# Optimization experiments

Hardware: AMD Instinct MI355X
Metric: run time of the kernel (lower is better)

The kernel has to match this reference:

```python
import jax, jax.numpy as jnp
import numpy as np

N_HEADS = 12
D_MODEL = 768
D_HEAD = 64
LN_EPS = 1e-5


def setup_inputs() -> dict:
    key = jax.random.key(0)
    ks = jax.random.split(key, 7)
    bs, slen = 1, 4096
    s_in = 1.0 / np.sqrt(D_MODEL)
    s_out = 1.0 / np.sqrt(N_HEADS * D_HEAD)
    return {
        "x": jax.random.normal(ks[0], (bs, slen, D_MODEL), jnp.float32),
        "W_attn": jax.random.uniform(ks[1], (D_MODEL, 3 * N_HEADS * D_HEAD), jnp.float32, -s_in, s_in),
        "b_attn": jax.random.uniform(ks[2], (3 * N_HEADS * D_HEAD,), jnp.float32, -s_in, s_in),
        "W_out": jax.random.uniform(ks[3], (N_HEADS * D_HEAD, D_MODEL), jnp.float32, -s_out, s_out),
        "b_out": jax.random.uniform(ks[4], (D_MODEL,), jnp.float32, -s_out, s_out),
        "ln_g": jnp.ones((D_MODEL,), jnp.float32),
        "ln_b": jnp.zeros((D_MODEL,), jnp.float32),
    }


def reference(x, W_attn, b_attn, W_out, b_out, ln_g, ln_b):
    bs, slen, _ = x.shape
    qkv = x @ W_attn + b_attn                      # [b, s, 3*H*D]
    wq, wk, wv = jnp.split(qkv, 3, axis=-1)
    def to_heads(t):
        return t.reshape(bs, slen, N_HEADS, D_HEAD)
    q, k, v = to_heads(wq), to_heads(wk), to_heads(wv)
    # scores: [b, h, s_q, s_k]
    scores = jnp.einsum('bqhd,bkhd->bhqk', q, k) / np.sqrt(D_HEAD).astype(np.float32)
    probs = jax.nn.softmax(scores, axis=-1)
    attn = jnp.einsum('bhqk,bkhd->bqhd', probs, v).reshape(bs, slen, N_HEADS * D_HEAD)
    out = attn @ W_out + b_out
    y = x + out
    mu = jnp.mean(y, axis=-1, keepdims=True)
    var = jnp.mean(jnp.square(y - mu), axis=-1, keepdims=True)
    return (y - mu) / jnp.sqrt(var + LN_EPS) * ln_g + ln_b
```

## Files before the change

### kernel.cpp

```cpp
#include <hip/hip_runtime.h>
#include <cstdint>
#include <cstddef>

#define SL 4096
#define DM 768

typedef short s16x8 __attribute__((ext_vector_type(8)));
typedef unsigned short u16x8 __attribute__((ext_vector_type(8)));
typedef unsigned short u16x4 __attribute__((ext_vector_type(4)));
typedef float f32x4 __attribute__((ext_vector_type(4)));
typedef float f32x16 __attribute__((ext_vector_type(16)));
typedef unsigned int u32x4 __attribute__((ext_vector_type(4)));

__device__ __forceinline__ unsigned short f2bf(float f) {
  unsigned u = __float_as_uint(f);
  u = u + 0x7fffu + ((u >> 16) & 1u);
  return (unsigned short)(u >> 16);
}

__device__ __forceinline__ int swz(int row, int col) {
  return (row << 6) + ((((col >> 3) ^ row) & 7) << 3) + (col & 7);
}

__device__ __forceinline__ int aswz(int row, int col) {
  return (row << 6) + ((((col >> 3) ^ row ^ (row >> 3)) & 7) << 3) + (col & 7);
}

__device__ __forceinline__ int vswz(int d, int col) {
  return (d << 5) + ((((col >> 3) ^ (d >> 1)) & 3) << 3) + (col & 7);
}

#define ASYNC16(G, L)                                                        \
  __builtin_amdgcn_global_load_lds(                                          \
      (const __attribute__((address_space(1))) void*)(G),                    \
      (__attribute__((address_space(3))) void*)(L), 16, 0, 0)

#define WAITB()                                   \
  do {                                            \
    asm volatile("s_waitcnt vmcnt(0)" ::: "memory"); \
    __builtin_amdgcn_s_barrier();                 \
  } while (0)

__device__ __forceinline__ void tr_body(
    const float* __restrict__ in, unsigned short* __restrict__ out,
    int R, int C, int bx, int by, float (*tile)[65], int t) {
  const int r0 = by * 64, c0 = bx * 64;
  const int lr = t >> 2, lcb = (t & 3) * 16;
  #pragma unroll
  for (int j = 0; j < 16; j += 4) {
    f32x4 v = *reinterpret_cast<const f32x4*>(in + (size_t)(r0 + lr) * C + c0 + lcb + j);
    tile[lr][lcb + j + 0] = v[0];
    tile[lr][lcb + j + 1] = v[1];
    tile[lr][lcb + j + 2] = v[2];
    tile[lr][lcb + j + 3] = v[3];
  }
  __syncthreads();
  #pragma unroll
  for (int j = 0; j < 16; j += 4) {
    u16x4 o;
    o[0] = f2bf(tile[lcb + j + 0][lr]);
    o[1] = f2bf(tile[lcb + j + 1][lr]);
    o[2] = f2bf(tile[lcb + j + 2][lr]);
    o[3] = f2bf(tile[lcb + j + 3][lr]);
    *reinterpret_cast<u16x4*>(out + (size_t)(c0 + lr) * R + r0 + lcb + j) = o;
  }
}

extern "C" __global__ __launch_bounds__(256) void k_prep(
    const float* __restrict__ x, const float* __restrict__ Wa,
    const float* __restrict__ Wo, unsigned short* __restrict__ xbf,
    unsigned short* __restrict__ wat, unsigned short* __restrict__ wot,
    unsigned* __restrict__ kmx) {
  __shared__ float tile[64][65];
  const int b = blockIdx.x, t = threadIdx.x;
  if (b < 3072) {
    if (b == 0 && t < 12) kmx[t] = 0u;
    const int i = (b * 256 + t) * 4;
    f32x4 v = *reinterpret_cast<const f32x4*>(x + i);
    u16x4 o;
    o[0] = f2bf(v[0]); o[1] = f2bf(v[1]); o[2] = f2bf(v[2]); o[3] = f2bf(v[3]);
    *reinterpret_cast<u16x4*>(xbf + i) = o;
  } else if (b < 3504) {
    const int bb = b - 3072;
    tr_body(Wa, wat, 768, 2304, bb % 36, bb / 36, tile, t);
  } else {
    const int bb = b - 3504;
    tr_body(Wo, wot, 768, 768, bb % 12, bb / 12, tile, t);
  }
}

extern "C" __global__ __launch_bounds__(256) void k_qkv(
    const unsigned short* __restrict__ xbf, const unsigned short* __restrict__ wt,
    const float* __restrict__ bias, unsigned short* __restrict__ qb,
    unsigned short* __restrict__ kbo, unsigned short* __restrict__ vtb,
    float* __restrict__ qn2, unsigned* __restrict__ kmx) {
  __shared__ alignas(16) unsigned short a_lds[2][8192];
  __shared__ alignas(16) unsigned short b_lds[2][8192];
  const int t = threadIdx.x, w = t >> 6, l = t & 63;
  const int l15 = l & 15, lg = l >> 4;
  const int wr = w >> 1, wc = w & 1;
  const int n0 = blockIdx.x * 128, m0 = blockIdx.y * 128;
  f32x4 acc[4][4];
  #pragma unroll
  for (int mt = 0; mt < 4; mt++)
    #pragma unroll
    for (int nt = 0; nt < 4; nt++) acc[mt][nt] = (f32x4)0.f;
  int soff[4];
  #pragma unroll
  for (int c = 0; c < 4; c++) {
    int i = c * 256 + t;
    int row = i >> 3, bp = i & 7;
    soff[c] = row * DM + (bp ^ (row & 7)) * 8;
  }
  const unsigned short* asrc = xbf + (size_t)m0 * DM;
  const unsigned short* bsrc = wt + (size_t)n0 * DM;

#define STAGE128(B, KK)                                                   \
  do {                                                                    \
    _Pragma("unroll")                                                     \
    for (int c = 0; c < 4; c++) {                                         \
      ASYNC16(asrc + (KK) + soff[c], &a_lds[B][0] + c * 2048 + w * 512);  \
      ASYNC16(bsrc + (KK) + soff[c], &b_lds[B][0] + c * 2048 + w * 512);  \
    }                                                                     \
  } while (0)

#define GEMM128(B)                                                            \
  do {                                                                        \
    _Pragma("unroll")                                                         \
    for (int kc = 0; kc < 2; kc++) {                                          \
      s16x8 af[4], bfv[4];                                                    \
      _Pragma("unroll")                                                       \
      for (int mt = 0; mt < 4; mt++)                                          \
        af[mt] = *reinterpret_cast<const s16x8*>(                             \
            &a_lds[B][swz(wr * 64 + mt * 16 + l15, kc * 32 + lg * 8)]);       \
      _Pragma("unroll")                                                       \
      for (int nt = 0; nt < 4; nt++)                                          \
        bfv[nt] = *reinterpret_cast<const s16x8*>(                            \
            &b_lds[B][swz(wc * 64 + nt * 16 + l15, kc * 32 + lg * 8)]);       \
      _Pragma("unroll")                                                       \
      for (int mt = 0; mt < 4; mt++)                                          \
        _Pragma("unroll")                                                     \
        for (int nt = 0; nt < 4; nt++)                                        \
          acc[mt][nt] = __builtin_amdgcn_mfma_f32_16x16x32_bf16(              \
              af[mt], bfv[nt], acc[mt][nt], 0, 0, 0);                         \
    }                                                                         \
  } while (0)

  STAGE128(0, 0);
  WAITB();
  #pragma unroll 1
  for (int kk = 0; kk < DM; kk += 128) {
    STAGE128(1, kk + 64);
    GEMM128(0);
    WAITB();
    if (kk + 128 < DM) STAGE128(0, kk + 128);
    GEMM128(1);
    WAITB();
  }
#undef STAGE128
#undef GEMM128

  const int secn = (n0 >= 1536) ? 2 : (n0 >= 768 ? 1 : 0);
  const int nbase = n0 - secn * 768 + wc * 64;
  const int h = nbase >> 6;
  const int mrow0 = m0 + wr * 64;
  float bv4[4];
  #pragma unroll
  for (int nt = 0; nt < 4; nt++) bv4[nt] = bias[secn * 768 + nbase + nt * 16 + l15];

  if (secn == 0) {
    const float QS = 0.180336880f;
    float s2[4][4];
    #pragma unroll
    for (int mt = 0; mt < 4; mt++) {
      #pragma unroll
      for (int r = 0; r < 4; r++) s2[mt][r] = 0.f;
    }
    #pragma unroll
    for (int mt = 0; mt < 4; mt++) {
      #pragma unroll
      for (int nt = 0; nt < 4; nt++) {
        const int d = nt * 16 + l15;
        #pragma unroll
        for (int r = 0; r < 4; r++) {
          const int m = mrow0 + mt * 16 + lg * 4 + r;
          float v = (acc[mt][nt][r] + bv4[nt]) * QS;
          qb[((size_t)h * SL + m) * 64 + d] = f2bf(v);
          s2[mt][r] = fmaf(v, v, s2[mt][r]);
        }
      }
    }
    #pragma unroll
    for (int mt = 0; mt < 4; mt++)
      #pragma unroll
      for (int r = 0; r < 4; r++) {
        #pragma unroll
        for (int off = 1; off < 16; off <<= 1)
          s2[mt][r] += __shfl_xor(s2[mt][r], off, 64);
      }
    if (l15 == 0) {
      #pragma unroll
      for (int mt = 0; mt < 4; mt++)
        #pragma unroll
        for (int r = 0; r < 4; r++)
          qn2[(size_t)h * SL + mrow0 + mt * 16 + lg * 4 + r] = s2[mt][r];
    }
  } else if (secn == 1) {
    float s2[4][4];
    #pragma unroll
    for (int mt = 0; mt < 4; mt++) {
      #pragma unroll
      for (int r = 0; r < 4; r++) s2[mt][r] = 0.f;
    }
    #pragma unroll
    for (int mt = 0; mt < 4; mt++) {
      #pragma unroll
      for (int nt = 0; nt < 4; nt++) {
        const int d = nt * 16 + l15;
        #pragma unroll
        for (int r = 0; r < 4; r++) {
          const int m = mrow0 + mt * 16 + lg * 4 + r;
          float v = acc[mt][nt][r] + bv4[nt];
          kbo[((size_t)h * SL + m) * 64 + d] = f2bf(v);
          s2[mt][r] = fmaf(v, v, s2[mt][r]);
        }
      }
    }
    float rm = 0.f;
    #pragma unroll
    for (int mt = 0; mt < 4; mt++)
      #pragma unroll
      for (int r = 0; r < 4; r++) {
        #pragma unroll
        for (int off = 1; off < 16; off <<= 1)
          s2[mt][r] += __shfl_xor(s2[mt][r], off, 64);
        rm = fmaxf(rm, s2[mt][r]);
      }
    rm = fmaxf(rm, __shfl_xor(rm, 16, 64));
    rm = fmaxf(rm, __shfl_xor(rm, 32, 64));
    if (l == 0) atomicMax(kmx + h, __float_as_uint(rm));
  } else {
    #pragma unroll
    for (int mt = 0; mt < 4; mt++) {
      #pragma unroll
      for (int nt = 0; nt < 4; nt++) {
        const int d = nt * 16 + l15;
        u16x4 o;
        #pragma unroll
        for (int r = 0; r < 4; r++) o[r] = f2bf(acc[mt][nt][r] + bv4[nt]);
        *reinterpret_cast<u16x4*>(
            vtb + ((size_t)h * 64 + d) * SL + mrow0 + mt * 16 + lg * 4) = o;
      }
    }
  }
}

__device__ __forceinline__ void attn_body32f(
    const unsigned short* kb, const unsigned short* vb,
    const s16x8* qf, f32x16* ot, f32x16& lacc, s16x8 qm,
    const int* kfo, const int* vfo, s16x8 ones) {
  f32x16 st = (f32x16)0.f;
  __builtin_amdgcn_s_setprio(1);
  #pragma unroll
  for (int c = 0; c < 4; c++) {
    s16x8 kf = *reinterpret_cast<const s16x8*>(&kb[kfo[c]]);
    st = __builtin_amdgcn_mfma_f32_32x32x16_bf16(kf, qf[c], st, 0, 0, 0);
  }
  st = __builtin_amdgcn_mfma_f32_32x32x16_bf16(ones, qm, st, 0, 0, 0);
  __builtin_amdgcn_s_setprio(0);
  #pragma unroll
  for (int r = 0; r < 16; r++) st[r] = exp2f(st[r]);
  #pragma unroll
  for (int m = 0; m < 2; m++) {
    const int m0 = m * 8;
    unsigned w0, w1, w2, w3;
    asm("v_cvt_pk_bf16_f32 %0, %1, %2" : "=v"(w0) : "v"(st[m0 + 0]), "v"(st[m0 + 1]));
    asm("v_cvt_pk_bf16_f32 %0, %1, %2" : "=v"(w1) : "v"(st[m0 + 2]), "v"(st[m0 + 3]));
    asm("v_cvt_pk_bf16_f32 %0, %1, %2" : "=v"(w2) : "v"(st[m0 + 4]), "v"(st[m0 + 5]));
    asm("v_cvt_pk_bf16_f32 %0, %1, %2" : "=v"(w3) : "v"(st[m0 + 6]), "v"(st[m0 + 7]));
    asm volatile("v_permlane32_swap_b32 %0, %1" : "+v"(w0), "+v"(w2));
    asm volatile("v_permlane32_swap_b32 %0, %1" : "+v"(w1), "+v"(w3));
    u32x4 wv_;
    wv_[0] = w0; wv_[1] = w1; wv_[2] = w2; wv_[3] = w3;
    s16x8 pbf = *reinterpret_cast<s16x8*>(&wv_);
    __builtin_amdgcn_s_setprio(1);
    #pragma unroll
    for (int dt = 0; dt < 2; dt++) {
      s16x8 vf = *reinterpret_cast<const s16x8*>(&vb[vfo[m * 2 + dt]]);
      ot[dt] = __builtin_amdgcn_mfma_f32_32x32x16_bf16(vf, pbf, ot[dt], 0, 0, 0);
    }
    lacc = __builtin_amdgcn_mfma_f32_32x32x16_bf16(ones, pbf, lacc, 0, 0, 0);
    __builtin_amdgcn_s_setprio(0);
  }
}

extern "C" __global__ __launch_bounds__(256) void k_attn(
    const unsigned short* __restrict__ qb, const unsigned short* __restrict__ kbi,
    const unsigned short* __restrict__ vt, const float* __restrict__ qn2,
    const unsigned* __restrict__ kmx, unsigned short* __restrict__ aout) {
  __shared__ alignas(16) unsigned char smem[32768];
  unsigned short* kst = (unsigned short*)smem;
  unsigned short* vst = (unsigned short*)(smem + 16384);
  const int t = threadIdx.x, w = t >> 6, l = t & 63;
  const int l31 = l & 31, s = l >> 5;
  const int half = w >> 1, qs = w & 1;
  const int bid = blockIdx.x;
  const int sid = (bid & 7) * 96 + (bid >> 3);
  const int h = sid >> 6, qt = sid & 63;
  const unsigned short* qh = qb + (size_t)h * SL * 64;
  const unsigned short* kh = kbi + (size_t)h * SL * 64 + (size_t)half * 2048 * 64;
  const unsigned short* vh = vt + (size_t)h * 64 * SL + half * 2048;
  const int q = qt * 64 + qs * 32 + l31;
  const float M = sqrtf(qn2[(size_t)h * SL + q] * __uint_as_float(kmx[h]));
  s16x8 qf[4];
  #pragma unroll
  for (int c = 0; c < 4; c++)
    qf[c] = *reinterpret_cast<const s16x8*>(qh + (size_t)q * 64 + c * 16 + s * 8);
  s16x8 ones;
  #pragma unroll
  for (int e = 0; e < 8; e++) ones[e] = (short)0x3F80;
  s16x8 qm = (s16x8)0;
  if (s == 0) qm[0] = (short)f2bf(-M);
  f32x16 ot[2];
  ot[0] = (f32x16)0.f;
  ot[1] = (f32x16)0.f;
  f32x16 lacc = (f32x16)0.f;
  int koff[2], voff[2];
  #pragma unroll
  for (int c = 0; c < 2; c++) {
    int i = (qs * 2 + c) * 64 + l;
    int key = i >> 3, kb_ = i & 7;
    koff[c] = key * 64 + (kb_ ^ ((key ^ (key >> 3)) & 7)) * 8;
    int d = i >> 2, vb_ = i & 3;
    voff[c] = d * SL + (vb_ ^ ((d >> 1) & 3)) * 8;
  }
  int kfo[4], vfo[4];
  #pragma unroll
  for (int c = 0; c < 4; c++) kfo[c] = aswz(l31, c * 16 + s * 8);
  #pragma unroll
  for (int m = 0; m < 2; m++)
    #pragma unroll
    for (int dt = 0; dt < 2; dt++) vfo[m * 2 + dt] = vswz(dt * 32 + l31, m * 16 + s * 8);

#define STAGE_KV(B, LB)                                                     \
  do {                                                                      \
    _Pragma("unroll")                                                       \
    for (int c = 0; c < 2; c++) {                                           \
      ASYNC16(kh + (size_t)(LB) * 64 + koff[c],                             \
              kst + (half * 2 + (B)) * 2048 + (qs * 2 + c) * 512);          \
      ASYNC16(vh + (LB) + voff[c],                                          \
              vst + (half * 2 + (B)) * 2048 + (qs * 2 + c) * 512);          \
    }                                                                       \
  } while (0)

  STAGE_KV(0, 0);
  WAITB();
  for (int lb = 0; lb < 2048; lb += 64) {
    STAGE_KV(1, lb + 32);
    attn_body32f(kst + (half * 2) * 2048, vst + (half * 2) * 2048,
                 qf, ot, lacc, qm, kfo, vfo, ones);
    WAITB();
    if (lb + 64 < 2048) STAGE_KV(0, lb + 64);
    attn_body32f(kst + (half * 2 + 1) * 2048, vst + (half * 2 + 1) * 2048,
                 qf, ot, lacc, qm, kfo, vfo, ones);
    WAITB();
  }
#undef STAGE_KV
  const float lsum = lacc[0];
  float* o_m = (float*)smem;
  float* l_m = (float*)(smem + 17408);
  __syncthreads();
  if (half == 1) {
    #pragma unroll
    for (int dt = 0; dt < 2; dt++) {
      #pragma unroll
      for (int rq = 0; rq < 4; rq++) {
        f32x4 v;
        #pragma unroll
        for (int j = 0; j < 4; j++) v[j] = ot[dt][rq * 4 + j];
        *reinterpret_cast<f32x4*>(&o_m[(qs * 32 + l31) * 68 + dt * 32 + rq * 8 + s * 4]) = v;
      }
    }
    if (s == 0) l_m[qs * 32 + l31] = lsum;
  }
  __syncthreads();
  if (half == 0) {
    const float linv = 1.f / (lsum + l_m[qs * 32 + l31]);
    #pragma unroll
    for (int dt = 0; dt < 2; dt++) {
      #pragma unroll
      for (int rq = 0; rq < 4; rq++) {
        f32x4 vb_ = *reinterpret_cast<const f32x4*>(&o_m[(qs * 32 + l31) * 68 + dt * 32 + rq * 8 + s * 4]);
        u16x4 o;
        #pragma unroll
        for (int j = 0; j < 4; j++)
          o[j] = f2bf((ot[dt][rq * 4 + j] + vb_[j]) * linv);
        *reinterpret_cast<u16x4*>(aout + (size_t)q * DM + h * 64 + dt * 32 + rq * 8 + s * 4) = o;
      }
    }
  }
}

__device__ __forceinline__ void gemm_body(
    const unsigned short* al, const unsigned short* bl, f32x4* acc,
    int wv, int l15, int lg) {
  #pragma unroll
  for (int kc = 0; kc < 2; kc++) {
    s16x8 af = *reinterpret_cast<const s16x8*>(&al[swz(wv * 16 + l15, kc * 32 + lg * 8)]);
    #pragma unroll
    for (int nt = 0; nt < 4; nt++) {
      s16x8 bfr = *reinterpret_cast<const s16x8*>(&bl[swz(nt * 16 + l15, kc * 32 + lg * 8)]);
      acc[nt] = __builtin_amdgcn_mfma_f32_16x16x32_bf16(af, bfr, acc[nt], 0, 0, 0);
    }
  }
}

extern "C" __global__ __launch_bounds__(256) void k_out(
    const unsigned short* __restrict__ abf, const unsigned short* __restrict__ wot,
    const float* __restrict__ bias, const float* __restrict__ x, float* __restrict__ y) {
  __shared__ alignas(16) unsigned short a_lds[2][4096];
  __shared__ alignas(16) unsigned short b_lds[2][4096];
  const int t = threadIdx.x, wv = t >> 6, l = t & 63;
  const int l15 = l & 15, lg = l >> 4;
  const int m0 = blockIdx.y * 64, n0 = blockIdx.x * 64;
  f32x4 acc[4];
  acc[0] = acc[1] = acc[2] = acc[3] = (f32x4)0.f;
  int soff[2];
  #pragma unroll
  for (int c = 0; c < 2; c++) {
    int idx = wv * 128 + c * 64 + l;
    int row = idx >> 3, bp = idx & 7;
    soff[c] = row * DM + (bp ^ (row & 7)) * 8;
  }
  const unsigned short* asrc = abf + (size_t)m0 * DM;
  const unsigned short* bsrc = wot + (size_t)n0 * DM;
  unsigned short* la = &a_lds[0][0];
  unsigned short* lb = &b_lds[0][0];

#define STAGE_AB(B, KK)                                              \
  do {                                                               \
    ASYNC16(asrc + (KK) + soff[0], la + (B)*4096 + wv * 1024);       \
    ASYNC16(asrc + (KK) + soff[1], la + (B)*4096 + wv * 1024 + 512); \
    ASYNC16(bsrc + (KK) + soff[0], lb + (B)*4096 + wv * 1024);       \
    ASYNC16(bsrc + (KK) + soff[1], lb + (B)*4096 + wv * 1024 + 512); \
  } while (0)

  STAGE_AB(0, 0);
  WAITB();
  for (int kk = 0; kk < DM; kk += 128) {
    STAGE_AB(1, kk + 64);
    gemm_body(&a_lds[0][0], &b_lds[0][0], acc, wv, l15, lg);
    WAITB();
    if (kk + 128 < DM) STAGE_AB(0, kk + 128);
    gemm_body(&a_lds[1][0], &b_lds[1][0], acc, wv, l15, lg);
    WAITB();
  }
#undef STAGE_AB
  const int mb = m0 + wv * 16 + lg * 4;
  #pragma unroll
  for (int nt = 0; nt < 4; nt++) {
    const int n = n0 + nt * 16 + l15;
    const float bv = bias[n];
    #pragma unroll
    for (int r = 0; r < 4; r++)
      y[(size_t)(mb + r) * DM + n] = acc[nt][r] + bv + x[(size_t)(mb + r) * DM + n];
  }
}

extern "C" __global__ __launch_bounds__(256) void k_ln(
    const float* __restrict__ y, const float* __restrict__ g, const float* __restrict__ b,
    float* __restrict__ out) {
  const int row = blockIdx.x, t = threadIdx.x;
  const float* yr = y + (size_t)row * DM;
  float v0 = yr[t], v1 = yr[t + 256], v2 = yr[t + 512];
  float sum = v0 + v1 + v2;
  float sq = v0 * v0 + v1 * v1 + v2 * v2;
  #pragma unroll
  for (int off = 1; off < 64; off <<= 1) {
    sum += __shfl_xor(sum, off, 64);
    sq += __shfl_xor(sq, off, 64);
  }
  __shared__ float ls[8];
  const int wv = t >> 6, l = t & 63;
  if (l == 0) { ls[wv] = sum; ls[4 + wv] = sq; }
  __syncthreads();
  sum = ls[0] + ls[1] + ls[2] + ls[3];
  sq = ls[4] + ls[5] + ls[6] + ls[7];
  const float mu = sum * (1.f / DM);
  const float rstd = rsqrtf(sq * (1.f / DM) - mu * mu + 1e-5f);
  out[(size_t)row * DM + t] = (v0 - mu) * rstd * g[t] + b[t];
  out[(size_t)row * DM + t + 256] = (v1 - mu) * rstd * g[t + 256] + b[t + 256];
  out[(size_t)row * DM + t + 512] = (v2 - mu) * rstd * g[t + 512] + b[t + 512];
}

extern "C" void kernel_launch(void* const* d_in, const int* in_sizes, int n_in,
                              void* d_out, int out_size, void* d_ws, size_t ws_size,
                              hipStream_t stream) {
  (void)in_sizes; (void)n_in; (void)out_size; (void)ws_size;
  const float* x = (const float*)d_in[0];
  const float* Wa = (const float*)d_in[1];
  const float* ba = (const float*)d_in[2];
  const float* Wo = (const float*)d_in[3];
  const float* bo = (const float*)d_in[4];
  const float* lng = (const float*)d_in[5];
  const float* lnb = (const float*)d_in[6];
  float* out = (float*)d_out;

  unsigned short* ws16 = (unsigned short*)d_ws;
  unsigned short* xbf = ws16;
  unsigned short* wat = xbf + 3145728;
  unsigned short* wot = wat + 1769472;
  unsigned short* qbf = wot + 589824;
  unsigned short* kbf = qbf + 3145728;
  unsigned short* vtb = kbf + 3145728;
  unsigned short* aob = vtb + 3145728;
  float* ybuf = (float*)(aob + 3145728);
  float* qn2 = ybuf + 3145728;
  unsigned* kmx = (unsigned*)(qn2 + 49152);

  k_prep<<<3648, 256, 0, stream>>>(x, Wa, Wo, xbf, wat, wot, kmx);
  k_qkv<<<dim3(18, 32), 256, 0, stream>>>(xbf, wat, ba, qbf, kbf, vtb, qn2, kmx);
  k_attn<<<768, 256, 0, stream>>>(qbf, kbf, vtb, qn2, kmx, aob);
  k_out<<<dim3(12, 64), 256, 0, stream>>>(aob, wot, bo, x, ybuf);
  k_ln<<<4096, 256, 0, stream>>>(ybuf, lng, lnb, out);
}
```

Before: 165.2 us.

## Load K/V fragments directly from global in attention; enlarge out-proj GEMM tiles

The attention kernel stops staging K and V tiles through LDS with async copies and barriers. Each wave now loads its MFMA fragments straight from global memory into registers and processes 64 keys per iteration. This removes the LDS round trip and the per-step barriers, at the cost of uncoalesced, redundant global/L2 reads and higher register pressure. Separately, the output-projection GEMM moves from 64x64 to 128x128 tiles with a 4x4 MFMA block per wave, which raises data reuse but shrinks the grid to 192 blocks.

```diff
diff --git a/kernel.cpp b/kernel.cpp
--- a/kernel.cpp
+++ b/kernel.cpp
@@ -20,14 +20,6 @@
 
 __device__ __forceinline__ int swz(int row, int col) {
   return (row << 6) + ((((col >> 3) ^ row) & 7) << 3) + (col & 7);
-}
-
-__device__ __forceinline__ int aswz(int row, int col) {
-  return (row << 6) + ((((col >> 3) ^ row ^ (row >> 3)) & 7) << 3) + (col & 7);
-}
-
-__device__ __forceinline__ int vswz(int d, int col) {
-  return (d << 5) + ((((col >> 3) ^ (d >> 1)) & 3) << 3) + (col & 7);
 }
 
 #define ASYNC16(G, L)                                                        \
@@ -255,52 +247,12 @@
   }
 }
 
-__device__ __forceinline__ void attn_body32f(
-    const unsigned short* kb, const unsigned short* vb,
-    const s16x8* qf, f32x16* ot, f32x16& lacc, s16x8 qm,
-    const int* kfo, const int* vfo, s16x8 ones) {
-  f32x16 st = (f32x16)0.f;
-  __builtin_amdgcn_s_setprio(1);
-  #pragma unroll
-  for (int c = 0; c < 4; c++) {
-    s16x8 kf = *reinterpret_cast<const s16x8*>(&kb[kfo[c]]);
-    st = __builtin_amdgcn_mfma_f32_32x32x16_bf16(kf, qf[c], st, 0, 0, 0);
-  }
-  st = __builtin_amdgcn_mfma_f32_32x32x16_bf16(ones, qm, st, 0, 0, 0);
-  __builtin_amdgcn_s_setprio(0);
-  #pragma unroll
-  for (int r = 0; r < 16; r++) st[r] = exp2f(st[r]);
-  #pragma unroll
-  for (int m = 0; m < 2; m++) {
-    const int m0 = m * 8;
-    unsigned w0, w1, w2, w3;
-    asm("v_cvt_pk_bf16_f32 %0, %1, %2" : "=v"(w0) : "v"(st[m0 + 0]), "v"(st[m0 + 1]));
-    asm("v_cvt_pk_bf16_f32 %0, %1, %2" : "=v"(w1) : "v"(st[m0 + 2]), "v"(st[m0 + 3]));
-    asm("v_cvt_pk_bf16_f32 %0, %1, %2" : "=v"(w2) : "v"(st[m0 + 4]), "v"(st[m0 + 5]));
-    asm("v_cvt_pk_bf16_f32 %0, %1, %2" : "=v"(w3) : "v"(st[m0 + 6]), "v"(st[m0 + 7]));
-    asm volatile("v_permlane32_swap_b32 %0, %1" : "+v"(w0), "+v"(w2));
-    asm volatile("v_permlane32_swap_b32 %0, %1" : "+v"(w1), "+v"(w3));
-    u32x4 wv_;
-    wv_[0] = w0; wv_[1] = w1; wv_[2] = w2; wv_[3] = w3;
-    s16x8 pbf = *reinterpret_cast<s16x8*>(&wv_);
-    __builtin_amdgcn_s_setprio(1);
-    #pragma unroll
-    for (int dt = 0; dt < 2; dt++) {
-      s16x8 vf = *reinterpret_cast<const s16x8*>(&vb[vfo[m * 2 + dt]]);
-      ot[dt] = __builtin_amdgcn_mfma_f32_32x32x16_bf16(vf, pbf, ot[dt], 0, 0, 0);
-    }
-    lacc = __builtin_amdgcn_mfma_f32_32x32x16_bf16(ones, pbf, lacc, 0, 0, 0);
-    __builtin_amdgcn_s_setprio(0);
-  }
-}
-
 extern "C" __global__ __launch_bounds__(256) void k_attn(
     const unsigned short* __restrict__ qb, const unsigned short* __restrict__ kbi,
     const unsigned short* __restrict__ vt, const float* __restrict__ qn2,
     const unsigned* __restrict__ kmx, unsigned short* __restrict__ aout) {
-  __shared__ alignas(16) unsigned char smem[32768];
-  unsigned short* kst = (unsigned short*)smem;
-  unsigned short* vst = (unsigned short*)(smem + 16384);
+  __shared__ float o_m[2][32][68];
+  __shared__ float l_m[2][32];
   const int t = threadIdx.x, w = t >> 6, l = t & 63;
   const int l31 = l & 31, s = l >> 5;
   const int half = w >> 1, qs = w & 1;
@@ -308,7 +260,7 @@
   const int sid = (bid & 7) * 96 + (bid >> 3);
   const int h = sid >> 6, qt = sid & 63;
   const unsigned short* qh = qb + (size_t)h * SL * 64;
-  const unsigned short* kh = kbi + (size_t)h * SL * 64 + (size_t)half * 2048 * 64;
+  const unsigned short* kh = kbi + ((size_t)h * SL + half * 2048) * 64;
   const unsigned short* vh = vt + (size_t)h * 64 * SL + half * 2048;
   const int q = qt * 64 + qs * 32 + l31;
   const float M = sqrtf(qn2[(size_t)h * SL + q] * __uint_as_float(kmx[h]));
@@ -321,55 +273,62 @@
   for (int e = 0; e < 8; e++) ones[e] = (short)0x3F80;
   s16x8 qm = (s16x8)0;
   if (s == 0) qm[0] = (short)f2bf(-M);
-  f32x16 ot[2];
-  ot[0] = (f32x16)0.f;
-  ot[1] = (f32x16)0.f;
-  f32x16 lacc = (f32x16)0.f;
-  int koff[2], voff[2];
-  #pragma unroll
-  for (int c = 0; c < 2; c++) {
-    int i = (qs * 2 + c) * 64 + l;
-    int key = i >> 3, kb_ = i & 7;
-    koff[c] = key * 64 + (kb_ ^ ((key ^ (key >> 3)) & 7)) * 8;
-    int d = i >> 2, vb_ = i & 3;
-    voff[c] = d * SL + (vb_ ^ ((d >> 1) & 3)) * 8;
-  }
-  int kfo[4], vfo[4];
-  #pragma unroll
-  for (int c = 0; c < 4; c++) kfo[c] = aswz(l31, c * 16 + s * 8);
-  #pragma unroll
-  for (int m = 0; m < 2; m++)
-    #pragma unroll
-    for (int dt = 0; dt < 2; dt++) vfo[m * 2 + dt] = vswz(dt * 32 + l31, m * 16 + s * 8);
-
-#define STAGE_KV(B, LB)                                                     \
-  do {                                                                      \
-    _Pragma("unroll")                                                       \
-    for (int c = 0; c < 2; c++) {                                           \
-      ASYNC16(kh + (size_t)(LB) * 64 + koff[c],                             \
-              kst + (half * 2 + (B)) * 2048 + (qs * 2 + c) * 512);          \
-      ASYNC16(vh + (LB) + voff[c],                                          \
-              vst + (half * 2 + (B)) * 2048 + (qs * 2 + c) * 512);          \
-    }                                                                       \
-  } while (0)
-
-  STAGE_KV(0, 0);
-  WAITB();
+  f32x16 ot0 = (f32x16)0.f, ot1 = (f32x16)0.f, lacc = (f32x16)0.f;
+  const int klane = l31 * 64 + s * 8;
+  const int vlane = l31 * SL + s * 8;
+
+  #pragma unroll 1
   for (int lb = 0; lb < 2048; lb += 64) {
-    STAGE_KV(1, lb + 32);
-    attn_body32f(kst + (half * 2) * 2048, vst + (half * 2) * 2048,
-                 qf, ot, lacc, qm, kfo, vfo, ones);
-    WAITB();
-    if (lb + 64 < 2048) STAGE_KV(0, lb + 64);
-    attn_body32f(kst + (half * 2 + 1) * 2048, vst + (half * 2 + 1) * 2048,
-                 qf, ot, lacc, qm, kfo, vfo, ones);
-    WAITB();
-  }
-#undef STAGE_KV
+    const unsigned short* kp = kh + (size_t)lb * 64 + klane;
+    s16x8 kf[2][4];
+    #pragma unroll
+    for (int kt = 0; kt < 2; kt++)
+      #pragma unroll
+      for (int c = 0; c < 4; c++)
+        kf[kt][c] = *reinterpret_cast<const s16x8*>(kp + kt * 2048 + c * 16);
+    f32x16 st0 = (f32x16)0.f, st1 = (f32x16)0.f;
+    __builtin_amdgcn_s_setprio(1);
+    #pragma unroll
+    for (int c = 0; c < 4; c++) {
+      st0 = __builtin_amdgcn_mfma_f32_32x32x16_bf16(kf[0][c], qf[c], st0, 0, 0, 0);
+      st1 = __builtin_amdgcn_mfma_f32_32x32x16_bf16(kf[1][c], qf[c], st1, 0, 0, 0);
+    }
+    st0 = __builtin_amdgcn_mfma_f32_32x32x16_bf16(ones, qm, st0, 0, 0, 0);
+    st1 = __builtin_amdgcn_mfma_f32_32x32x16_bf16(ones, qm, st1, 0, 0, 0);
+    __builtin_amdgcn_s_setprio(0);
+    const unsigned short* vp = vh + lb + vlane;
+    s16x8 vf[2][4];
+    #pragma unroll
+    for (int dt = 0; dt < 2; dt++)
+      #pragma unroll
+      for (int cc = 0; cc < 4; cc++)
+        vf[dt][cc] = *reinterpret_cast<const s16x8*>(vp + dt * 32 * SL + cc * 16);
+    #pragma unroll
+    for (int r = 0; r < 16; r++) st0[r] = exp2f(st0[r]);
+    #pragma unroll
+    for (int r = 0; r < 16; r++) st1[r] = exp2f(st1[r]);
+    #pragma unroll
+    for (int cc = 0; cc < 4; cc++) {
+      const int m0 = (cc & 1) * 8;
+      const f32x16& stk = (cc < 2) ? st0 : st1;
+      unsigned w0, w1, w2, w3;
+      asm("v_cvt_pk_bf16_f32 %0, %1, %2" : "=v"(w0) : "v"(stk[m0 + 0]), "v"(stk[m0 + 1]));
+      asm("v_cvt_pk_bf16_f32 %0, %1, %2" : "=v"(w1) : "v"(stk[m0 + 2]), "v"(stk[m0 + 3]));
+      asm("v_cvt_pk_bf16_f32 %0, %1, %2" : "=v"(w2) : "v"(stk[m0 + 4]), "v"(stk[m0 + 5]));
+      asm("v_cvt_pk_bf16_f32 %0, %1, %2" : "=v"(w3) : "v"(stk[m0 + 6]), "v"(stk[m0 + 7]));
+      asm volatile("v_permlane32_swap_b32 %0, %1" : "+v"(w0), "+v"(w2));
+      asm volatile("v_permlane32_swap_b32 %0, %1" : "+v"(w1), "+v"(w3));
+      u32x4 wv_;
+      wv_[0] = w0; wv_[1] = w1; wv_[2] = w2; wv_[3] = w3;
+      s16x8 pbf = *reinterpret_cast<s16x8*>(&wv_);
+      __builtin_amdgcn_s_setprio(1);
+      ot0 = __builtin_amdgcn_mfma_f32_32x32x16_bf16(vf[0][cc], pbf, ot0, 0, 0, 0);
+      ot1 = __builtin_amdgcn_mfma_f32_32x32x16_bf16(vf[1][cc], pbf, ot1, 0, 0, 0);
+      lacc = __builtin_amdgcn_mfma_f32_32x32x16_bf16(ones, pbf, lacc, 0, 0, 0);
+      __builtin_amdgcn_s_setprio(0);
+    }
+  }
   const float lsum = lacc[0];
-  float* o_m = (float*)smem;
-  float* l_m = (float*)(smem + 17408);
-  __syncthreads();
   if (half == 1) {
     #pragma unroll
     for (int dt = 0; dt < 2; dt++) {
@@ -377,40 +336,26 @@
       for (int rq = 0; rq < 4; rq++) {
         f32x4 v;
         #pragma unroll
-        for (int j = 0; j < 4; j++) v[j] = ot[dt][rq * 4 + j];
-        *reinterpret_cast<f32x4*>(&o_m[(qs * 32 + l31) * 68 + dt * 32 + rq * 8 + s * 4]) = v;
-      }
-    }
-    if (s == 0) l_m[qs * 32 + l31] = lsum;
+        for (int j = 0; j < 4; j++) v[j] = (dt ? ot1 : ot0)[rq * 4 + j];
+        *reinterpret_cast<f32x4*>(&o_m[qs][l31][dt * 32 + rq * 8 + s * 4]) = v;
+      }
+    }
+    if (s == 0) l_m[qs][l31] = lsum;
   }
   __syncthreads();
   if (half == 0) {
-    const float linv = 1.f / (lsum + l_m[qs * 32 + l31]);
+    const float linv = 1.f / (lsum + l_m[qs][l31]);
     #pragma unroll
     for (int dt = 0; dt < 2; dt++) {
       #pragma unroll
       for (int rq = 0; rq < 4; rq++) {
-        f32x4 vb_ = *reinterpret_cast<const f32x4*>(&o_m[(qs * 32 + l31) * 68 + dt * 32 + rq * 8 + s * 4]);
+        f32x4 vb_ = *reinterpret_cast<const f32x4*>(&o_m[qs][l31][dt * 32 + rq * 8 + s * 4]);
         u16x4 o;
         #pragma unroll
         for (int j = 0; j < 4; j++)
-          o[j] = f2bf((ot[dt][rq * 4 + j] + vb_[j]) * linv);
+          o[j] = f2bf(((dt ? ot1 : ot0)[rq * 4 + j] + vb_[j]) * linv);
         *reinterpret_cast<u16x4*>(aout + (size_t)q * DM + h * 64 + dt * 32 + rq * 8 + s * 4) = o;
       }
-    }
-  }
-}
-
-__device__ __forceinline__ void gemm_body(
-    const unsigned short* al, const unsigned short* bl, f32x4* acc,
-    int wv, int l15, int lg) {
-  #pragma unroll
-  for (int kc = 0; kc < 2; kc++) {
-    s16x8 af = *reinterpret_cast<const s16x8*>(&al[swz(wv * 16 + l15, kc * 32 + lg * 8)]);
-    #pragma unroll
-    for (int nt = 0; nt < 4; nt++) {
-      s16x8 bfr = *reinterpret_cast<const s16x8*>(&bl[swz(nt * 16 + l15, kc * 32 + lg * 8)]);
-      acc[nt] = __builtin_amdgcn_mfma_f32_16x16x32_bf16(af, bfr, acc[nt], 0, 0, 0);
     }
   }
 }
@@ -418,52 +363,85 @@
 extern "C" __global__ __launch_bounds__(256) void k_out(
     const unsigned short* __restrict__ abf, const unsigned short* __restrict__ wot,
     const float* __restrict__ bias, const float* __restrict__ x, float* __restrict__ y) {
-  __shared__ alignas(16) unsigned short a_lds[2][4096];
-  __shared__ alignas(16) unsigned short b_lds[2][4096];
-  const int t = threadIdx.x, wv = t >> 6, l = t & 63;
+  __shared__ alignas(16) unsigned short a_lds[2][8192];
+  __shared__ alignas(16) unsigned short b_lds[2][8192];
+  const int t = threadIdx.x, w = t >> 6, l = t & 63;
   const int l15 = l & 15, lg = l >> 4;
-  const int m0 = blockIdx.y * 64, n0 = blockIdx.x * 64;
-  f32x4 acc[4];
-  acc[0] = acc[1] = acc[2] = acc[3] = (f32x4)0.f;
-  int soff[2];
-  #pragma unroll
-  for (int c = 0; c < 2; c++) {
-    int idx = wv * 128 + c * 64 + l;
-    int row = idx >> 3, bp = idx & 7;
+  const int wr = w >> 1, wc = w & 1;
+  const int n0 = blockIdx.x * 128, m0 = blockIdx.y * 128;
+  f32x4 acc[4][4];
+  #pragma unroll
+  for (int mt = 0; mt < 4; mt++)
+    #pragma unroll
+    for (int nt = 0; nt < 4; nt++) acc[mt][nt] = (f32x4)0.f;
+  int soff[4];
+  #pragma unroll
+  for (int c = 0; c < 4; c++) {
+    int i = c * 256 + t;
+    int row = i >> 3, bp = i & 7;
     soff[c] = row * DM + (bp ^ (row & 7)) * 8;
   }
   const unsigned short* asrc = abf + (size_t)m0 * DM;
   const unsigned short* bsrc = wot + (size_t)n0 * DM;
-  unsigned short* la = &a_lds[0][0];
-  unsigned short* lb = &b_lds[0][0];
-
-#define STAGE_AB(B, KK)                                              \
-  do {                                                               \
-    ASYNC16(asrc + (KK) + soff[0], la + (B)*4096 + wv * 1024);       \
-    ASYNC16(asrc + (KK) + soff[1], la + (B)*4096 + wv * 1024 + 512); \
-    ASYNC16(bsrc + (KK) + soff[0], lb + (B)*4096 + wv * 1024);       \
-    ASYNC16(bsrc + (KK) + soff[1], lb + (B)*4096 + wv * 1024 + 512); \
+
+#define STAGE128(B, KK)                                                   \
+  do {                                                                    \
+    _Pragma("unroll")                                                     \
+    for (int c = 0; c < 4; c++) {                                         \
+      ASYNC16(asrc + (KK) + soff[c], &a_lds[B][0] + c * 2048 + w * 512);  \
+      ASYNC16(bsrc + (KK) + soff[c], &b_lds[B][0] + c * 2048 + w * 512);  \
+    }                                                                     \
   } while (0)
 
-  STAGE_AB(0, 0);
+#define GEMM128(B)                                                            \
+  do {                                                                        \
+    _Pragma("unroll")                                                         \
+    for (int kc = 0; kc < 2; kc++) {                                          \
+      s16x8 af[4], bfv[4];                                                    \
+      _Pragma("unroll")                                                       \
+      for (int mt = 0; mt < 4; mt++)                                          \
+        af[mt] = *reinterpret_cast<const s16x8*>(                             \
+            &a_lds[B][swz(wr * 64 + mt * 16 + l15, kc * 32 + lg * 8)]);       \
+      _Pragma("unroll")                                                       \
+      for (int nt = 0; nt < 4; nt++)                                          \
+        bfv[nt] = *reinterpret_cast<const s16x8*>(                            \
+            &b_lds[B][swz(wc * 64 + nt * 16 + l15, kc * 32 + lg * 8)]);       \
+      _Pragma("unroll")                                                       \
+      for (int mt = 0; mt < 4; mt++)                                          \
+        _Pragma("unroll")                                                     \
+        for (int nt = 0; nt < 4; nt++)                                        \
+          acc[mt][nt] = __builtin_amdgcn_mfma_f32_16x16x32_bf16(              \
+              af[mt], bfv[nt], acc[mt][nt], 0, 0, 0);                         \
+    }                                                                         \
+  } while (0)
+
+  STAGE128(0, 0);
   WAITB();
+  #pragma unroll 1
   for (int kk = 0; kk < DM; kk += 128) {
-    STAGE_AB(1, kk + 64);
-    gemm_body(&a_lds[0][0], &b_lds[0][0], acc, wv, l15, lg);
+    STAGE128(1, kk + 64);
+    GEMM128(0);
     WAITB();
-    if (kk + 128 < DM) STAGE_AB(0, kk + 128);
-    gemm_body(&a_lds[1][0], &b_lds[1][0], acc, wv, l15, lg);
+    if (kk + 128 < DM) STAGE128(0, kk + 128);
+    GEMM128(1);
     WAITB();
   }
-#undef STAGE_AB
-  const int mb = m0 + wv * 16 + lg * 4;
+#undef STAGE128
+#undef GEMM128
+
+  const int mrow0 = m0 + wr * 64;
   #pragma unroll
   for (int nt = 0; nt < 4; nt++) {
-    const int n = n0 + nt * 16 + l15;
+    const int n = n0 + wc * 64 + nt * 16 + l15;
     const float bv = bias[n];
     #pragma unroll
-    for (int r = 0; r < 4; r++)
-      y[(size_t)(mb + r) * DM + n] = acc[nt][r] + bv + x[(size_t)(mb + r) * DM + n];
+    for (int mt = 0; mt < 4; mt++) {
+      #pragma unroll
+      for (int r = 0; r < 4; r++) {
+        const int m = mrow0 + mt * 16 + lg * 4 + r;
+        y[(size_t)m * DM + n] = acc[mt][nt][r] + bv + x[(size_t)m * DM + n];
+      }
+    }
   }
 }
 
@@ -521,6 +499,6 @@
   k_prep<<<3648, 256, 0, stream>>>(x, Wa, Wo, xbf, wat, wot, kmx);
   k_qkv<<<dim3(18, 32), 256, 0, stream>>>(xbf, wat, ba, qbf, kbf, vtb, qn2, kmx);
   k_attn<<<768, 256, 0, stream>>>(qbf, kbf, vtb, qn2, kmx, aob);
-  k_out<<<dim3(12, 64), 256, 0, stream>>>(aob, wot, bo, x, ybuf);
+  k_out<<<dim3(6, 32), 256, 0, stream>>>(aob, wot, bo, x, ybuf);
   k_ln<<<4096, 256, 0, stream>>>(ybuf, lng, lnb, out);
 }
```

Result: slower. 253.1 us (+53.2%).

## Overlap KV staging using partial vmcnt waits and unify K/V LDS swizzle

Applied to the files above, without the earlier changes.

The attention loop now waits with vmcnt(4) before each single barrier, instead of draining all loads with two full waits and barriers per half-iteration. This lets the next K/V tile's global-to-LDS copy stay in flight during compute. The V tile LDS layout is remapped to 64-element rows so K and V share one XOR swizzle, and the fragment offsets are computed more cheaply. The catch is a possible race: a buffer can be re-staged while the sibling wave may still be reading it, because the barrier that followed compute was removed.

```diff
diff --git a/kernel.cpp b/kernel.cpp
--- a/kernel.cpp
+++ b/kernel.cpp
@@ -22,14 +22,6 @@
   return (row << 6) + ((((col >> 3) ^ row) & 7) << 3) + (col & 7);
 }
 
-__device__ __forceinline__ int aswz(int row, int col) {
-  return (row << 6) + ((((col >> 3) ^ row ^ (row >> 3)) & 7) << 3) + (col & 7);
-}
-
-__device__ __forceinline__ int vswz(int d, int col) {
-  return (d << 5) + ((((col >> 3) ^ (d >> 1)) & 3) << 3) + (col & 7);
-}
-
 #define ASYNC16(G, L)                                                        \
   __builtin_amdgcn_global_load_lds(                                          \
       (const __attribute__((address_space(1))) void*)(G),                    \
@@ -40,6 +32,8 @@
     asm volatile("s_waitcnt vmcnt(0)" ::: "memory"); \
     __builtin_amdgcn_s_barrier();                 \
   } while (0)
+
+#define MF32(A, B, C) __builtin_amdgcn_mfma_f32_32x32x16_bf16((A), (B), (C), 0, 0, 0)
 
 __device__ __forceinline__ void tr_body(
     const float* __restrict__ in, unsigned short* __restrict__ out,
@@ -264,9 +258,9 @@
   #pragma unroll
   for (int c = 0; c < 4; c++) {
     s16x8 kf = *reinterpret_cast<const s16x8*>(&kb[kfo[c]]);
-    st = __builtin_amdgcn_mfma_f32_32x32x16_bf16(kf, qf[c], st, 0, 0, 0);
-  }
-  st = __builtin_amdgcn_mfma_f32_32x32x16_bf16(ones, qm, st, 0, 0, 0);
+    st = MF32(kf, qf[c], st);
+  }
+  st = MF32(ones, qm, st);
   __builtin_amdgcn_s_setprio(0);
   #pragma unroll
   for (int r = 0; r < 16; r++) st[r] = exp2f(st[r]);
@@ -287,9 +281,9 @@
     #pragma unroll
     for (int dt = 0; dt < 2; dt++) {
       s16x8 vf = *reinterpret_cast<const s16x8*>(&vb[vfo[m * 2 + dt]]);
-      ot[dt] = __builtin_amdgcn_mfma_f32_32x32x16_bf16(vf, pbf, ot[dt], 0, 0, 0);
-    }
-    lacc = __builtin_amdgcn_mfma_f32_32x32x16_bf16(ones, pbf, lacc, 0, 0, 0);
+      ot[dt] = MF32(vf, pbf, ot[dt]);
+    }
+    lacc = MF32(ones, pbf, lacc);
     __builtin_amdgcn_s_setprio(0);
   }
 }
@@ -308,7 +302,7 @@
   const int sid = (bid & 7) * 96 + (bid >> 3);
   const int h = sid >> 6, qt = sid & 63;
   const unsigned short* qh = qb + (size_t)h * SL * 64;
-  const unsigned short* kh = kbi + (size_t)h * SL * 64 + (size_t)half * 2048 * 64;
+  const unsigned short* kh = kbi + ((size_t)h * SL + half * 2048) * 64;
   const unsigned short* vh = vt + (size_t)h * 64 * SL + half * 2048;
   const int q = qt * 64 + qs * 32 + l31;
   const float M = sqrtf(qn2[(size_t)h * SL + q] * __uint_as_float(kmx[h]));
@@ -329,18 +323,21 @@
   #pragma unroll
   for (int c = 0; c < 2; c++) {
     int i = (qs * 2 + c) * 64 + l;
-    int key = i >> 3, kb_ = i & 7;
-    koff[c] = key * 64 + (kb_ ^ ((key ^ (key >> 3)) & 7)) * 8;
-    int d = i >> 2, vb_ = i & 3;
-    voff[c] = d * SL + (vb_ ^ ((d >> 1) & 3)) * 8;
-  }
+    int row = i >> 3, sb = i & 7;
+    int bp = sb ^ ((row ^ (row >> 3)) & 7);
+    koff[c] = row * 64 + bp * 8;
+    int d = row + 32 * (bp >> 2);
+    voff[c] = d * SL + (bp & 3) * 8;
+  }
+  const int sr = (l31 ^ (l31 >> 3)) & 7;
   int kfo[4], vfo[4];
   #pragma unroll
-  for (int c = 0; c < 4; c++) kfo[c] = aswz(l31, c * 16 + s * 8);
+  for (int c = 0; c < 4; c++) kfo[c] = (l31 << 6) + (((c * 2 + s) ^ sr) << 3);
   #pragma unroll
   for (int m = 0; m < 2; m++)
     #pragma unroll
-    for (int dt = 0; dt < 2; dt++) vfo[m * 2 + dt] = vswz(dt * 32 + l31, m * 16 + s * 8);
+    for (int dt = 0; dt < 2; dt++)
+      vfo[m * 2 + dt] = (l31 << 6) + (((dt * 4 + m * 2 + s) ^ sr) << 3);
 
 #define STAGE_KV(B, LB)                                                     \
   do {                                                                      \
@@ -354,16 +351,22 @@
   } while (0)
 
   STAGE_KV(0, 0);
-  WAITB();
+  #pragma unroll 1
   for (int lb = 0; lb < 2048; lb += 64) {
     STAGE_KV(1, lb + 32);
+    asm volatile("s_waitcnt vmcnt(4)" ::: "memory");
+    __builtin_amdgcn_s_barrier();
     attn_body32f(kst + (half * 2) * 2048, vst + (half * 2) * 2048,
                  qf, ot, lacc, qm, kfo, vfo, ones);
-    WAITB();
-    if (lb + 64 < 2048) STAGE_KV(0, lb + 64);
+    if (lb + 64 < 2048) {
+      STAGE_KV(0, lb + 64);
+      asm volatile("s_waitcnt vmcnt(4)" ::: "memory");
+    } else {
+      asm volatile("s_waitcnt vmcnt(0)" ::: "memory");
+    }
+    __builtin_amdgcn_s_barrier();
     attn_body32f(kst + (half * 2 + 1) * 2048, vst + (half * 2 + 1) * 2048,
                  qf, ot, lacc, qm, kfo, vfo, ones);
-    WAITB();
   }
 #undef STAGE_KV
   const float lsum = lacc[0];
```

Measured after the change: 164.7 us. About the same (-0.3%).
